# Performance work log

Hardware: AMD Instinct MI355X
Metric: run time of the kernel (lower is better)

The kernel has to match this reference:

```python
import jax, jax.numpy as jnp
import numpy as np
from jax import lax

SCORE_THRESHOLD = 0.02
IOU_THRESHOLD = 0.5
NUM_CLASSES = 80
MAX_DETECTIONS = 10  # tf.image.non_max_suppression max_output_size in the source
ANCHORS = np.array([[1.08, 1.19], [3.42, 4.41], [6.63, 11.38], [9.42, 5.11], [16.62, 10.52]], dtype=np.float32)


def setup_inputs() -> dict:
    key = jax.random.key(0)
    k1, _ = jax.random.split(key)
    B, H, W = 16, 76, 76
    A = ANCHORS.shape[0]
    feats = jax.random.normal(k1, (B, H, W, A * (5 + NUM_CLASSES)), dtype=jnp.float32)
    anchors = jnp.asarray(ANCHORS)
    return {"feats": feats, "anchors": anchors}


def yolo_head(feats, anchors, num_classes):
    """Standard YOLOv2 decode (interpret_prediction)."""
    B, H, W, _ = feats.shape
    A = anchors.shape[0]
    feats = feats.reshape(B, H, W, A, 5 + num_classes)
    gy, gx = jnp.meshgrid(jnp.arange(H), jnp.arange(W), indexing="ij")
    grid = jnp.stack([gx, gy], axis=-1).astype(feats.dtype)  # [H,W,2] in (x,y) order
    conv_dims = jnp.array([W, H], dtype=feats.dtype)
    box_xy = (jax.nn.sigmoid(feats[..., 0:2]) + grid[None, :, :, None, :]) / conv_dims
    box_wh = jnp.exp(feats[..., 2:4]) * anchors[None, None, None, :, :] / conv_dims
    box_confidence = jax.nn.sigmoid(feats[..., 4:5])
    box_class_probs = jax.nn.softmax(feats[..., 5:], axis=-1)
    return box_xy, box_wh, box_confidence, box_class_probs


def _postprocess(feats, anchors):
    box_xy, box_wh, box_confidence, box_class_probs = yolo_head(feats, anchors, NUM_CLASSES)
    box_mins = box_xy - box_wh / 2.0
    box_maxes = box_xy + box_wh / 2.0
    # [y_min, x_min, y_max, x_max] as in the source (indices 1 then 0)
    boxes = jnp.concatenate([box_mins[..., 1:2], box_mins[..., 0:1], box_maxes[..., 1:2], box_maxes[..., 0:1]], axis=-1)
    box_scores = box_confidence * box_class_probs           # [B,H,W,A,C]
    box_classes = jnp.argmax(box_scores, axis=-1)           # [B,H,W,A]
    box_class_scores = jnp.max(box_scores, axis=-1)         # [B,H,W,A]

    # tf.boolean_mask flattens across all dims; emulate with fixed shapes by
    # marking below-threshold candidates as invalid (score -1).
    flat_boxes = boxes.reshape(-1, 4)                       # [N,4]
    flat_scores = box_class_scores.reshape(-1)              # [N]
    flat_classes = box_classes.reshape(-1)                  # [N]
    scores_work = jnp.where(flat_scores >= SCORE_THRESHOLD, flat_scores, -1.0)

    N = flat_boxes.shape[0]
    areas = jnp.maximum(flat_boxes[:, 2] - flat_boxes[:, 0], 0.0) * jnp.maximum(flat_boxes[:, 3] - flat_boxes[:, 1], 0.0)
    idx_range = jnp.arange(N)

    def step(sw, _):
        idx = jnp.argmax(sw)
        s = sw[idx]
        valid = s >= SCORE_THRESHOLD
        box = flat_boxes[idx]                               # [4] = y1,x1,y2,x2
        iy1 = jnp.maximum(box[0], flat_boxes[:, 0])
        ix1 = jnp.maximum(box[1], flat_boxes[:, 1])
        iy2 = jnp.minimum(box[2], flat_boxes[:, 2])
        ix2 = jnp.minimum(box[3], flat_boxes[:, 3])
        inter = jnp.maximum(iy2 - iy1, 0.0) * jnp.maximum(ix2 - ix1, 0.0)
        box_area = jnp.maximum(box[2] - box[0], 0.0) * jnp.maximum(box[3] - box[1], 0.0)
        iou = inter / (box_area + areas - inter + 1e-9)
        suppress = (iou > IOU_THRESHOLD) | (idx_range == idx)
        sw_new = jnp.where(valid & suppress, -1.0, sw)
        row = jnp.concatenate([box, s[None], flat_classes[idx].astype(jnp.float32)[None]])  # [6]
        row = jnp.where(valid, row, jnp.zeros_like(row))
        return sw_new, row

    _, rows = lax.scan(step, scores_work, None, length=MAX_DETECTIONS)
    return rows  # [MAX_DETECTIONS, 6] = [y1,x1,y2,x2,score,class]; zero rows are padding


def reference(feats, anchors):
    return _postprocess(feats, anchors)
```

## Files before the change

### kernel.cpp

```cpp
#include <hip/hip_runtime.h>
#include <stdint.h>

#define N_CAND 462080
#define NBINS  2048
#define HIST_BLOCKS 32
#define COMPACT_BLOCKS 64
#define TARGET 256u
#define SMAX   1024
#define SCORE_THR 0.02f
#define NT 14440
#define TILEF 2720
#define C_CNT 0
#define C_BIN 16
#define C_HD  32
#define C_CD  48


typedef const __attribute__((address_space(1))) uint32_t* gas1_u32;
typedef __attribute__((address_space(3))) uint32_t*       las3_u32;
#define GLOAD_LDS16(g, l) __builtin_amdgcn_global_load_lds( \
    (gas1_u32)(const void*)(g), (las3_u32)(void*)(l), 16, 0, 0)

__global__ __launch_bounds__(64) void decode_kernel(
    const float* __restrict__ feats,
    float* __restrict__ scores, unsigned int* __restrict__ ctrl)
{
    __shared__ __align__(16) float lds[TILEF];
    const int t = threadIdx.x;
    const int c = t & 31;
    const int h = t >> 5;
    const int tile = blockIdx.x;

    if (tile == 0 && t == 0) { ctrl[C_HD] = 0u; ctrl[C_CD] = 0u; }

    {
        const float4* __restrict__ src = (const float4*)(feats + (size_t)tile * TILEF);
        float4* dst = (float4*)lds;
#pragma unroll
        for (int i = 0; i < 10; ++i)
            GLOAD_LDS16(src + i * 64 + t, dst + i * 64 + t);
        if (t < 40) GLOAD_LDS16(src + 640 + t, dst + 640 + t);
    }
    asm volatile("s_waitcnt vmcnt(0)" ::: "memory");
    __builtin_amdgcn_sched_barrier(0);

    const float* f = lds + c * 85;
    const int kb = 5 + h * 40;

    float m0 = f[kb + 0], m1 = f[kb + 1], m2 = f[kb + 2], m3 = f[kb + 3];
#pragma unroll
    for (int k = 4; k < 40; k += 4) {
        m0 = fmaxf(m0, f[kb + k + 0]);
        m1 = fmaxf(m1, f[kb + k + 1]);
        m2 = fmaxf(m2, f[kb + k + 2]);
        m3 = fmaxf(m3, f[kb + k + 3]);
    }
    float mloc = fmaxf(fmaxf(m0, m1), fmaxf(m2, m3));
    float mall = fmaxf(mloc, __shfl_xor(mloc, 32));

    float s0 = 0.f, s1 = 0.f, s2 = 0.f, s3 = 0.f;
#pragma unroll
    for (int k = 0; k < 40; k += 4) {
        s0 += __expf(f[kb + k + 0] - mall);
        s1 += __expf(f[kb + k + 1] - mall);
        s2 += __expf(f[kb + k + 2] - mall);
        s3 += __expf(f[kb + k + 3] - mall);
    }
    float sl = (s0 + s1) + (s2 + s3);
    float sall = sl + __shfl_xor(sl, 32);

    if (h == 0) {
        float conf = 1.0f / (1.0f + __expf(-f[4]));
        float score = conf / sall;
        scores[tile * 32 + c] = (score >= SCORE_THR) ? score : -1.0f;
    }
}

__global__ __launch_bounds__(1024) void hist_cutoff_kernel(
    const float* __restrict__ scores, unsigned short* __restrict__ hist_part,
    unsigned int* __restrict__ ctrl)
{
    __shared__ unsigned int lh[NBINS];
    __shared__ unsigned int pa[1024], pb[1024];
    __shared__ int lastf;
    const int t = threadIdx.x;

    lh[2 * t] = 0u; lh[2 * t + 1] = 0u;
    __syncthreads();

    for (int i = blockIdx.x * 1024 + t; i < N_CAND; i += HIST_BLOCKS * 1024) {
        float s = scores[i];
        if (s >= SCORE_THR) {
            int bin = (int)(s * (float)NBINS);
            bin = bin > (NBINS - 1) ? (NBINS - 1) : bin;
            atomicAdd(&lh[bin], 1u);
        }
    }
    __syncthreads();
    unsigned int* outp = (unsigned int*)(hist_part + (size_t)blockIdx.x * NBINS);
    outp[t] = (lh[2 * t] & 0xFFFFu) | (lh[2 * t + 1] << 16);
    __syncthreads();

    if (t == 0) {
        __threadfence();
        unsigned old = atomicAdd(&ctrl[C_HD], 1u);
        lastf = (old == HIST_BLOCKS - 1) ? 1 : 0;
    }
    __syncthreads();
    if (!lastf) return;
    if (t == 0) __threadfence();
    __syncthreads();

    const unsigned int* hp32 = (const unsigned int*)hist_part;
    unsigned b0 = 0u, b1 = 0u;
#pragma unroll 4
    for (int p = 0; p < HIST_BLOCKS; ++p) {
        unsigned v = hp32[p * 1024 + t];
        b0 += v & 0xFFFFu;
        b1 += v >> 16;
    }
    lh[2 * t] = b0; lh[2 * t + 1] = b1;
    pa[t] = b0 + b1;
    __syncthreads();

    unsigned int* srcb = pa; unsigned int* dstb = pb;
    for (int off = 1; off < 1024; off <<= 1) {
        unsigned v = srcb[t] + ((t + off < 1024) ? srcb[t + off] : 0u);
        dstb[t] = v;
        __syncthreads();
        unsigned int* tmp = srcb; srcb = dstb; dstb = tmp;
    }
    unsigned St = srcb[t];
    unsigned Sn = (t < 1023) ? srcb[t + 1] : 0u;

    if (t == 0) {
        ctrl[C_CNT] = 0u;
        if (St < TARGET) ctrl[C_BIN] = 0u;
    }
    if (St >= TARGET && Sn < TARGET) {
        unsigned run = Sn + lh[2 * t + 1];
        ctrl[C_BIN] = (run >= TARGET) ? (unsigned)(2 * t + 1) : (unsigned)(2 * t);
    }
}

__device__ inline float4 decode_box(const float* __restrict__ feats,
                                    const float* __restrict__ anchors, int ci)
{
    int a = ci % 5;
    int cell = ci / 5;
    int gx = cell % 76;
    int gy = (cell / 76) % 76;
    const float* f = feats + (long long)ci * 85;
    float bx = (1.0f / (1.0f + __expf(-f[0])) + (float)gx) / 76.0f;
    float by = (1.0f / (1.0f + __expf(-f[1])) + (float)gy) / 76.0f;
    float bw = __expf(f[2]) * anchors[2 * a]     / 76.0f;
    float bh = __expf(f[3]) * anchors[2 * a + 1] / 76.0f;
    return make_float4(by - bh * 0.5f, bx - bw * 0.5f,
                       by + bh * 0.5f, bx + bw * 0.5f);
}

__global__ __launch_bounds__(1024) void compact_nms_kernel(
    const float* __restrict__ scores, unsigned int* __restrict__ ctrl,
    float* __restrict__ lscore, int* __restrict__ lidx,
    const float* __restrict__ feats, const float* __restrict__ anchors,
    float* __restrict__ out)
{
    __shared__ unsigned long long wkey[16];
    __shared__ unsigned long long bkey;
    __shared__ float4 bbox;
    __shared__ int lastf;
    const int t = threadIdx.x;

    const int cut = (int)ctrl[C_BIN];
    for (int i = blockIdx.x * 1024 + t; i < N_CAND; i += COMPACT_BLOCKS * 1024) {
        float sw = scores[i];
        if (sw >= SCORE_THR) {
            int bin = (int)(sw * (float)NBINS);
            bin = bin > (NBINS - 1) ? (NBINS - 1) : bin;
            if (bin >= cut) {
                unsigned pos = atomicAdd(&ctrl[C_CNT], 1u);
                if (pos < SMAX) { lscore[pos] = sw; lidx[pos] = i; }
            }
        }
    }
    __syncthreads();
    if (t == 0) {
        __threadfence();
        unsigned old = atomicAdd(&ctrl[C_CD], 1u);
        lastf = (old == COMPACT_BLOCKS - 1) ? 1 : 0;
    }
    __syncthreads();
    if (!lastf) return;
    if (t == 0) __threadfence();
    __syncthreads();

    unsigned cnt = ctrl[C_CNT];
    int n = (cnt < (unsigned)SMAX) ? (int)cnt : SMAX;

    unsigned long long key = 0ull;
    float4 mb = make_float4(0.f, 0.f, 0.f, 0.f);
    float  msc = 0.f, mcls = 0.f;
    unsigned midx = 0xFFFFFFFFu;
    bool aliveb = false;
    if (t < n) {
        msc  = lscore[t];
        midx = (unsigned)lidx[t];
        key  = ((unsigned long long)__float_as_uint(msc) << 32)
             | (unsigned long long)(0xFFFFFFFFu - midx);
        mb   = decode_box(feats, anchors, (int)midx);
        const float* fc = feats + (size_t)midx * 85 + 5;
        float bm = fc[0]; int cb = 0;
#pragma unroll 4
        for (int k = 1; k < 80; ++k) {
            float v = fc[k];
            if (v > bm) { bm = v; cb = k; }
        }
        mcls = (float)cb;
        aliveb = true;
    }

    for (int r = 0; r < 10; ++r) {
        unsigned long long k0 = aliveb ? key : 0ull;
#pragma unroll
        for (int msk = 32; msk > 0; msk >>= 1) {
            unsigned long long o = __shfl_xor(k0, msk);
            k0 = (o > k0) ? o : k0;
        }
        if ((t & 63) == 0) wkey[t >> 6] = k0;
        __syncthreads();
        if (t < 16) {
            unsigned long long v = wkey[t];
#pragma unroll
            for (int msk = 8; msk > 0; msk >>= 1) {
                unsigned long long o = __shfl_xor(v, msk);
                v = (o > v) ? o : v;
            }
            if (t == 0) bkey = v;
        }
        __syncthreads();

        unsigned long long wk = bkey;
        bool have = (wk != 0ull);
        unsigned widx = have ? (0xFFFFFFFFu - (unsigned)(wk & 0xFFFFFFFFull)) : 0xFFFFFFFFu;

        if (have && aliveb && midx == widx) {
            bbox = mb;
            out[r * 6 + 0] = mb.x;
            out[r * 6 + 1] = mb.y;
            out[r * 6 + 2] = mb.z;
            out[r * 6 + 3] = mb.w;
            out[r * 6 + 4] = msc;
            out[r * 6 + 5] = mcls;
            aliveb = false;
        }
        if (!have && t == 0) {
#pragma unroll
            for (int q = 0; q < 6; ++q) out[r * 6 + q] = 0.f;
        }
        __syncthreads();

        if (have && aliveb) {
            float4 ab = bbox;
            float aarea = fmaxf(ab.z - ab.x, 0.f) * fmaxf(ab.w - ab.y, 0.f);
            float iy1 = fmaxf(ab.x, mb.x);
            float ix1 = fmaxf(ab.y, mb.y);
            float iy2 = fminf(ab.z, mb.z);
            float ix2 = fminf(ab.w, mb.w);
            float inter = fmaxf(iy2 - iy1, 0.f) * fmaxf(ix2 - ix1, 0.f);
            float carea = fmaxf(mb.z - mb.x, 0.f) * fmaxf(mb.w - mb.y, 0.f);
            float iou = inter / (aarea + carea - inter + 1e-9f);
            if (iou > 0.5f) aliveb = false;
        }
    }
}

extern "C" void kernel_launch(void* const* d_in, const int* in_sizes, int n_in,
                              void* d_out, int out_size, void* d_ws, size_t ws_size,
                              hipStream_t stream) {
    const float* feats   = (const float*)d_in[0];
    const float* anchors = (const float*)d_in[1];
    char* ws = (char*)d_ws;

    unsigned int*   ctrl      = (unsigned int*)(ws + 0);
    unsigned short* hist_part = (unsigned short*)(ws + 256);
    float*          lscore    = (float*)(ws + 131328);
    int*            lidx      = (int*)(ws + 135424);
    float*          scores    = (float*)(ws + 139520);
    float*          out       = (float*)d_out;

    decode_kernel      <<<NT, 64, 0, stream>>>(feats, scores, ctrl);
    hist_cutoff_kernel <<<HIST_BLOCKS, 1024, 0, stream>>>(scores, hist_part, ctrl);
    compact_nms_kernel <<<COMPACT_BLOCKS, 1024, 0, stream>>>(scores, ctrl, lscore, lidx,
                                                             feats, anchors, out);
}
```

Before: 70.01 us.

## Compute class argmax in decode and process two candidate tiles per block

```diff
diff --git a/kernel.cpp b/kernel.cpp
--- a/kernel.cpp
+++ b/kernel.cpp
@@ -8,8 +8,7 @@
 #define TARGET 256u
 #define SMAX   1024
 #define SCORE_THR 0.02f
-#define NT 14440
-#define TILEF 2720
+#define NB 7220
 #define C_CNT 0
 #define C_BIN 16
 #define C_HD  32
@@ -23,56 +22,73 @@
 
 __global__ __launch_bounds__(64) void decode_kernel(
     const float* __restrict__ feats,
-    float* __restrict__ scores, unsigned int* __restrict__ ctrl)
+    float* __restrict__ scores, unsigned char* __restrict__ cls,
+    unsigned int* __restrict__ ctrl)
 {
-    __shared__ __align__(16) float lds[TILEF];
+    __shared__ __align__(16) float lds[64 * 85];
     const int t = threadIdx.x;
     const int c = t & 31;
     const int h = t >> 5;
-    const int tile = blockIdx.x;
-
-    if (tile == 0 && t == 0) { ctrl[C_HD] = 0u; ctrl[C_CD] = 0u; }
+
+    if (blockIdx.x == 0 && t == 0) { ctrl[C_HD] = 0u; ctrl[C_CD] = 0u; }
 
     {
-        const float4* __restrict__ src = (const float4*)(feats + (size_t)tile * TILEF);
+        const float4* __restrict__ src = (const float4*)(feats + (size_t)blockIdx.x * 5440);
         float4* dst = (float4*)lds;
 #pragma unroll
         for (int i = 0; i < 10; ++i)
             GLOAD_LDS16(src + i * 64 + t, dst + i * 64 + t);
         if (t < 40) GLOAD_LDS16(src + 640 + t, dst + 640 + t);
-    }
-    asm volatile("s_waitcnt vmcnt(0)" ::: "memory");
-    __builtin_amdgcn_sched_barrier(0);
-
-    const float* f = lds + c * 85;
-    const int kb = 5 + h * 40;
-
-    float m0 = f[kb + 0], m1 = f[kb + 1], m2 = f[kb + 2], m3 = f[kb + 3];
-#pragma unroll
-    for (int k = 4; k < 40; k += 4) {
-        m0 = fmaxf(m0, f[kb + k + 0]);
-        m1 = fmaxf(m1, f[kb + k + 1]);
-        m2 = fmaxf(m2, f[kb + k + 2]);
-        m3 = fmaxf(m3, f[kb + k + 3]);
-    }
-    float mloc = fmaxf(fmaxf(m0, m1), fmaxf(m2, m3));
-    float mall = fmaxf(mloc, __shfl_xor(mloc, 32));
-
-    float s0 = 0.f, s1 = 0.f, s2 = 0.f, s3 = 0.f;
-#pragma unroll
-    for (int k = 0; k < 40; k += 4) {
-        s0 += __expf(f[kb + k + 0] - mall);
-        s1 += __expf(f[kb + k + 1] - mall);
-        s2 += __expf(f[kb + k + 2] - mall);
-        s3 += __expf(f[kb + k + 3] - mall);
-    }
-    float sl = (s0 + s1) + (s2 + s3);
-    float sall = sl + __shfl_xor(sl, 32);
-
-    if (h == 0) {
-        float conf = 1.0f / (1.0f + __expf(-f[4]));
-        float score = conf / sall;
-        scores[tile * 32 + c] = (score >= SCORE_THR) ? score : -1.0f;
+#pragma unroll
+        for (int i = 0; i < 10; ++i)
+            GLOAD_LDS16(src + 680 + i * 64 + t, dst + 680 + i * 64 + t);
+        if (t < 40) GLOAD_LDS16(src + 1320 + t, dst + 1320 + t);
+    }
+
+#pragma unroll
+    for (int half = 0; half < 2; ++half) {
+        if (half == 0)
+            asm volatile("s_waitcnt vmcnt(11)" ::: "memory");
+        else
+            asm volatile("s_waitcnt vmcnt(0)" ::: "memory");
+        __builtin_amdgcn_sched_barrier(0);
+
+        const int cand = half * 32 + c;
+        const float* f = lds + cand * 85;
+        const int kb = 5 + h * 40;
+
+        float m = f[kb];
+        int cb = h * 40;
+#pragma unroll
+        for (int k = 1; k < 40; ++k) {
+            float v = f[kb + k];
+            if (v > m) { m = v; cb = h * 40 + k; }
+        }
+        float mo = __shfl_xor(m, 32);
+        int   cbo = __shfl_xor(cb, 32);
+        float m0 = (h == 0) ? m : mo,  m1 = (h == 0) ? mo : m;
+        int   c0 = (h == 0) ? cb : cbo, c1 = (h == 0) ? cbo : cb;
+        float mall = fmaxf(m0, m1);
+        int   cls_abs = (m0 >= m1) ? c0 : c1;
+
+        float s0 = 0.f, s1 = 0.f, s2 = 0.f, s3 = 0.f;
+#pragma unroll
+        for (int k = 0; k < 40; k += 4) {
+            s0 += __expf(f[kb + k + 0] - mall);
+            s1 += __expf(f[kb + k + 1] - mall);
+            s2 += __expf(f[kb + k + 2] - mall);
+            s3 += __expf(f[kb + k + 3] - mall);
+        }
+        float sl = (s0 + s1) + (s2 + s3);
+        float sall = sl + __shfl_xor(sl, 32);
+
+        if (h == 0) {
+            const int ci = blockIdx.x * 64 + cand;
+            float conf = 1.0f / (1.0f + __expf(-f[4]));
+            float score = conf / sall;
+            scores[ci] = (score >= SCORE_THR) ? score : -1.0f;
+            cls[ci] = (unsigned char)cls_abs;
+        }
     }
 }
 
@@ -163,7 +179,7 @@
     const float* __restrict__ scores, unsigned int* __restrict__ ctrl,
     float* __restrict__ lscore, int* __restrict__ lidx,
     const float* __restrict__ feats, const float* __restrict__ anchors,
-    float* __restrict__ out)
+    const unsigned char* __restrict__ cls, float* __restrict__ out)
 {
     __shared__ unsigned long long wkey[16];
     __shared__ unsigned long long bkey;
@@ -208,14 +224,7 @@
         key  = ((unsigned long long)__float_as_uint(msc) << 32)
              | (unsigned long long)(0xFFFFFFFFu - midx);
         mb   = decode_box(feats, anchors, (int)midx);
-        const float* fc = feats + (size_t)midx * 85 + 5;
-        float bm = fc[0]; int cb = 0;
-#pragma unroll 4
-        for (int k = 1; k < 80; ++k) {
-            float v = fc[k];
-            if (v > bm) { bm = v; cb = k; }
-        }
-        mcls = (float)cb;
+        mcls = (float)cls[midx];
         aliveb = true;
     }
 
@@ -286,10 +295,11 @@
     float*          lscore    = (float*)(ws + 131328);
     int*            lidx      = (int*)(ws + 135424);
     float*          scores    = (float*)(ws + 139520);
+    unsigned char*  cls       = (unsigned char*)(ws + 1987840);
     float*          out       = (float*)d_out;
 
-    decode_kernel      <<<NT, 64, 0, stream>>>(feats, scores, ctrl);
+    decode_kernel      <<<NB, 64, 0, stream>>>(feats, scores, cls, ctrl);
     hist_cutoff_kernel <<<HIST_BLOCKS, 1024, 0, stream>>>(scores, hist_part, ctrl);
     compact_nms_kernel <<<COMPACT_BLOCKS, 1024, 0, stream>>>(scores, ctrl, lscore, lidx,
-                                                             feats, anchors, out);
-}
+                                                             feats, anchors, cls, out);
+}
```

New measurement: 59.76 us. 1.17x faster.
